# Kernel optimization log

Measured on AMD Instinct MI355X. Metric: run time of the kernel, lower is better.

The kernel has to match this reference:

```python
import jax, jax.numpy as jnp
import numpy as np

ROPE_BASE = 10000.0


def _apply_rope(q, k, start_pos):
    # q, k: (B, T, H, D) with half-split (LLaMA-style) rotation
    B, T, H, D = q.shape
    half = D // 2
    inv_freq = 1.0 / (ROPE_BASE ** (jnp.arange(0, half, dtype=jnp.float32) / half))
    pos = (start_pos + jnp.arange(T)).astype(jnp.float32)
    ang = pos[:, None] * inv_freq[None, :]          # (T, half)
    cos = jnp.cos(ang)[None, :, None, :]            # (1, T, 1, half)
    sin = jnp.sin(ang)[None, :, None, :]

    def rot(t):
        t1, t2 = t[..., :half], t[..., half:]
        return jnp.concatenate([t1 * cos - t2 * sin, t1 * sin + t2 * cos], axis=-1)

    return rot(q), rot(k)


def setup_inputs() -> dict:
    key = jax.random.key(0)
    k1, k2, k3 = jax.random.split(key, 3)
    B, T, C = 2, 2048, 2048
    x = jax.random.normal(k1, (B, T, C), dtype=jnp.float32)
    # torch Linear weights: (out_features, in_features), scaled like default init
    Wqkv = jax.random.normal(k2, (3 * C, C), dtype=jnp.float32) * (C ** -0.5)
    Wproj = jax.random.normal(k3, (C, C), dtype=jnp.float32) * (C ** -0.5)
    return {"x": x, "Wqkv": Wqkv, "Wproj": Wproj, "start_pos": 0}


def reference(x, Wqkv, Wproj, start_pos):
    B, T, C = x.shape
    H = 16
    D = C // H
    scale = D ** -0.5

    qkv = x @ Wqkv.T                                 # (B, T, 3C)
    q, k, v = jnp.split(qkv, 3, axis=-1)
    q = q.reshape(B, T, H, D)
    k = k.reshape(B, T, H, D)
    v = v.reshape(B, T, H, D)
    q, k = _apply_rope(q, k, start_pos)

    att = jnp.einsum("bthd,bshd->bhts", q, k) * scale   # (B, H, T, T)
    causal = jnp.tril(jnp.ones((T, T), dtype=bool))
    att = jnp.where(causal[None, None], att, -jnp.inf)
    att = jax.nn.softmax(att, axis=-1)
    out = jnp.einsum("bhts,bshd->bthd", att, v)          # (B, T, H, D)
    out = out.reshape(B, T, C)
    return out @ Wproj.T
```

## Files before the change

kernel.cpp:

```cpp
#include <hip/hip_runtime.h>
#include <hip/hip_bf16.h>
#include <stdint.h>
#include <math.h>

#define B_    2
#define T_    2048
#define C_    2048
#define H_    16
#define D_    128
#define NQKV  6144
#define BT_   4096

typedef __attribute__((ext_vector_type(8))) short  short8;
typedef __attribute__((ext_vector_type(4))) short  short4_;
typedef __attribute__((ext_vector_type(4))) float  float4_;

__device__ __forceinline__ unsigned short f2bf(float f) {
  union { float f; unsigned int u; } v; v.f = f;
  unsigned int u = v.u;
  return (unsigned short)((u + 0x7FFFu + ((u >> 16) & 1u)) >> 16);
}
__device__ __forceinline__ float bf2f(unsigned short u) {
  union { unsigned int i; float f; } v; v.i = ((unsigned int)u) << 16;
  return v.f;
}
__device__ __forceinline__ void pk2(short4_& dst, int idx2, float a, float b) {
  union { __hip_bfloat162 h2; struct { short x, y; } s; } u;
  u.h2 = __float22bfloat162_rn(make_float2(a, b));
  dst[idx2 * 2]     = u.s.x;
  dst[idx2 * 2 + 1] = u.s.y;
}

__device__ __forceinline__ void async_cp16(const unsigned short* g, unsigned short* l) {
  __builtin_amdgcn_global_load_lds((__attribute__((address_space(1))) void*)g,
                                   (__attribute__((address_space(3))) void*)l,
                                   16, 0, 0);
}

__global__ __launch_bounds__(256) void cvt_all(const float* __restrict__ x,
                                               const float* __restrict__ wqkv,
                                               const float* __restrict__ wproj,
                                               unsigned short* __restrict__ out) {
  int i = (blockIdx.x * 256 + threadIdx.x) * 8;
  const float* src; int off;
  if (i < 8388608)       { src = x;     off = i; }
  else if (i < 20971520) { src = wqkv;  off = i - 8388608; }
  else                   { src = wproj; off = i - 20971520; }
  const float4_* p = (const float4_*)(src + off);
  float4_ a = p[0], b = p[1];
  short8 o;
  o[0] = (short)f2bf(a[0]); o[1] = (short)f2bf(a[1]);
  o[2] = (short)f2bf(a[2]); o[3] = (short)f2bf(a[3]);
  o[4] = (short)f2bf(b[0]); o[5] = (short)f2bf(b[1]);
  o[6] = (short)f2bf(b[2]); o[7] = (short)f2bf(b[3]);
  *(short8*)(out + i) = o;
}

template <bool F32OUT>
__global__ __launch_bounds__(256) void gemm_bt(const unsigned short* __restrict__ A,
                                               const unsigned short* __restrict__ Bm,
                                               void* __restrict__ Cout,
                                               int M, int N, int K) {
  __shared__ __align__(16) unsigned short As[128 * 64];
  __shared__ __align__(16) unsigned short Bs[128 * 64];
  const int tid  = threadIdx.x;
  const int lane = tid & 63;
  const int col16 = lane & 15, quad = lane >> 4;
  const int wave = tid >> 6;
  const int wm = wave >> 1, wn = wave & 1;
  const int m0 = blockIdx.y * 128, n0 = blockIdx.x * 128;

  float4_ acc[4][4] = {};

  #pragma unroll 1
  for (int k0 = 0; k0 < K; k0 += 64) {
    __syncthreads();
    #pragma unroll
    for (int i = 0; i < 4; ++i) {
      int P   = i * 256 + tid;
      int row = P >> 3;
      int kc  = (P & 7) ^ (row & 7);
      async_cp16(A  + (size_t)(m0 + row) * K + k0 + kc * 8, As + P * 8);
      async_cp16(Bm + (size_t)(n0 + row) * K + k0 + kc * 8, Bs + P * 8);
    }
    __syncthreads();
    #pragma unroll
    for (int ks = 0; ks < 2; ++ks) {
      short8 af[4], bf[4];
      #pragma unroll
      for (int i = 0; i < 4; ++i) {
        int ra = wm * 64 + i * 16 + col16;
        int ca = ((ks * 4 + quad) ^ (ra & 7)) * 8;
        af[i] = *(const short8*)(As + ra * 64 + ca);
        int rb = wn * 64 + i * 16 + col16;
        int cb = ((ks * 4 + quad) ^ (rb & 7)) * 8;
        bf[i] = *(const short8*)(Bs + rb * 64 + cb);
      }
      #pragma unroll
      for (int i = 0; i < 4; ++i)
        #pragma unroll
        for (int j = 0; j < 4; ++j)
          acc[i][j] = __builtin_amdgcn_mfma_f32_16x16x32_bf16(af[i], bf[j], acc[i][j], 0, 0, 0);
    }
  }

  #pragma unroll
  for (int i = 0; i < 4; ++i) {
    int mg = m0 + wm * 64 + i * 16 + quad * 4;
    #pragma unroll
    for (int j = 0; j < 4; ++j) {
      int ng = n0 + wn * 64 + j * 16 + col16;
      #pragma unroll
      for (int r = 0; r < 4; ++r) {
        if constexpr (F32OUT)
          ((float*)Cout)[(size_t)(mg + r) * N + ng] = acc[i][j][r];
        else
          ((unsigned short*)Cout)[(size_t)(mg + r) * N + ng] = f2bf(acc[i][j][r]);
      }
    }
  }
}

__global__ __launch_bounds__(256) void rope_split(const unsigned short* __restrict__ qkv,
                                                  const int* __restrict__ sp_ptr,
                                                  unsigned short* __restrict__ q_r,
                                                  unsigned short* __restrict__ k_r,
                                                  unsigned short* __restrict__ v_t) {
  __shared__ __align__(16) unsigned short vs[128 * 64];
  const int blk  = blockIdx.x;
  const int bh   = blk >> 5;
  const int tile = blk & 31;
  const int b = bh >> 4, h = bh & 15;
  const int t0 = tile * 64;
  const int tid = threadIdx.x;
  const int qidx = tid & 15;
  const int sp = sp_ptr[0];
  const bool hi = (qidx & 8) != 0;
  const float L2F = -0.20762050593046013f;
  const float SCL = 0.1275174117f;

  #pragma unroll
  for (int p = 0; p < 4; ++p) {
    int row = p * 16 + (tid >> 4);
    int tg  = t0 + row;
    size_t base = (size_t)(b * T_ + tg) * NQKV + h * D_ + qidx * 8;
    short8 q8 = *(const short8*)(qkv + base);
    short8 k8 = *(const short8*)(qkv + base + 2048);
    short8 v8 = *(const short8*)(qkv + base + 4096);
    float qf[8], kf[8], qp[8], kp[8];
    #pragma unroll
    for (int j = 0; j < 8; ++j) { qf[j] = bf2f((unsigned short)q8[j]); kf[j] = bf2f((unsigned short)k8[j]); }
    #pragma unroll
    for (int j = 0; j < 8; ++j) { qp[j] = __shfl_xor(qf[j], 8); kp[j] = __shfl_xor(kf[j], 8); }
    float pos = (float)(sp + tg);
    short8 qo, ko;
    #pragma unroll
    for (int j = 0; j < 8; ++j) {
      int d  = qidx * 8 + j;
      int fi = d & 63;
      float freq = exp2f((float)fi * L2F);
      float ang = pos * freq;
      float s = sinf(ang), c = cosf(ang);
      float sq = s * SCL, cq = c * SCL;
      float o1 = hi ? (qp[j] * sq + qf[j] * cq) : (qf[j] * cq - qp[j] * sq);
      float o2 = hi ? (kp[j] * s  + kf[j] * c ) : (kf[j] * c  - kp[j] * s );
      qo[j] = (short)f2bf(o1);
      ko[j] = (short)f2bf(o2);
    }
    size_t ob = (size_t)(bh * T_ + tg) * D_ + qidx * 8;
    *(short8*)(q_r + ob) = qo;
    *(short8*)(k_r + ob) = ko;
    #pragma unroll
    for (int j = 0; j < 8; ++j) {
      int d  = qidx * 8 + j;
      int prc = (row >> 3) ^ ((d >> 3) & 7);
      vs[d * 64 + prc * 8 + (row & 7)] = (unsigned short)v8[j];
    }
  }
  __syncthreads();
  int drow = tid >> 1;
  int half = tid & 1;
  size_t gb = (size_t)(bh * D_ + drow) * T_ + t0 + half * 32;
  #pragma unroll
  for (int c = 0; c < 4; ++c) {
    int rc  = half * 4 + c;
    int prc = rc ^ ((drow >> 3) & 7);
    *(short8*)(v_t + gb + c * 8) = *(const short8*)(vs + drow * 64 + prc * 8);
  }
}

__global__ __launch_bounds__(512) void attn_fwd(const unsigned short* __restrict__ q_r,
                                                const unsigned short* __restrict__ k_r,
                                                const unsigned short* __restrict__ v_t,
                                                unsigned short* __restrict__ Ob) {
  __shared__ __align__(16) unsigned short Ks[2][64 * 128];
  __shared__ __align__(16) unsigned short Vts[2][128 * 64];
  __shared__ __align__(16) unsigned short Ps[128 * 64];
  const int pairb = blockIdx.x >> 5;
  const int bh    = blockIdx.x & 31;
  const int tid  = threadIdx.x;
  const int lane = tid & 63;
  const int col16 = lane & 15, quad = lane >> 4;
  const int wave = tid >> 6;
  const float NEG_INF = -__builtin_inff();
  const int b = bh >> 4, h = bh & 15;
  const int qlr = wave * 16 + col16;

  #pragma unroll 1
  for (int half = 0; half < 2; ++half) {
    const int qt = half ? (15 - pairb) : pairb;
    const int q0 = qt * 128;
    const int njt = 2 * qt + 2;

    short8 qf[4];
    const unsigned short* qp = q_r + (size_t)(bh * T_ + q0 + qlr) * D_;
    #pragma unroll
    for (int ks = 0; ks < 4; ++ks) qf[ks] = *(const short8*)(qp + ks * 32 + quad * 8);

    float4_ oacc[8] = {};
    float m_i = NEG_INF, l_i = 0.f;

    __syncthreads();

    const unsigned short* kbase = k_r + (size_t)bh * T_ * D_;
    const unsigned short* vbase = v_t + (size_t)bh * D_ * T_;
    #define STAGE(JT, BUF)                                                        \
      {                                                                           \
        const unsigned short* kb = kbase + (size_t)(JT) * 64 * D_;                \
        const unsigned short* vb = vbase + (size_t)(JT) * 64;                     \
        unsigned short* kd = &Ks[(BUF)][0];                                       \
        unsigned short* vd = &Vts[(BUF)][0];                                      \
        _Pragma("unroll")                                                         \
        for (int i = 0; i < 2; ++i) {                                             \
          int P = i * 512 + tid;                                                  \
          int krow = P >> 4, kc = (P & 15) ^ (krow & 7);                          \
          async_cp16(kb + krow * D_ + kc * 8, kd + P * 8);                        \
          int vrow = P >> 3, vc = (P & 7) ^ (vrow & 7);                           \
          async_cp16(vb + (size_t)vrow * T_ + vc * 8, vd + P * 8);                \
        }                                                                         \
      }

    STAGE(0, 0);

    #pragma unroll 1
    for (int jt = 0; jt < njt; ++jt) {
      __syncthreads();
      if (jt + 1 < njt) STAGE(jt + 1, (jt + 1) & 1);

      if (jt * 64 > q0 + wave * 16 + 15) continue;

      const unsigned short* KsB  = &Ks[jt & 1][0];
      const unsigned short* VtsB = &Vts[jt & 1][0];

      float4_ s[4];
      #pragma unroll
      for (int jn = 0; jn < 4; ++jn) {
        float4_ a = {};
        #pragma unroll
        for (int ks = 0; ks < 4; ++ks) {
          int kr = jn * 16 + col16;
          int ch = ((ks * 4 + quad) ^ (kr & 7)) * 8;
          short8 kfr = *(const short8*)(KsB + kr * 128 + ch);
          a = __builtin_amdgcn_mfma_f32_16x16x32_bf16(kfr, qf[ks], a, 0, 0, 0);
        }
        s[jn] = a;
      }
      if (jt * 64 + 63 > q0 + wave * 16) {
        #pragma unroll
        for (int jn = 0; jn < 4; ++jn)
          #pragma unroll
          for (int r = 0; r < 4; ++r)
            if (jt * 64 + jn * 16 + quad * 4 + r > q0 + qlr) s[jn][r] = NEG_INF;
      }
      float rm = NEG_INF;
      #pragma unroll
      for (int jn = 0; jn < 4; ++jn)
        #pragma unroll
        for (int r = 0; r < 4; ++r) rm = fmaxf(rm, s[jn][r]);
      rm = fmaxf(rm, __shfl_xor(rm, 16));
      rm = fmaxf(rm, __shfl_xor(rm, 32));
      float m_new = fmaxf(m_i, rm);
      float alpha = exp2f(m_i - m_new);
      float rs = 0.f;
      #pragma unroll
      for (int jn = 0; jn < 4; ++jn)
        #pragma unroll
        for (int r = 0; r < 4; ++r) {
          float pv = exp2f(s[jn][r] - m_new);
          s[jn][r] = pv;
          rs += pv;
        }
      rs += __shfl_xor(rs, 16);
      rs += __shfl_xor(rs, 32);
      l_i = l_i * alpha + rs;
      m_i = m_new;
      #pragma unroll
      for (int dt = 0; dt < 8; ++dt) oacc[dt] *= alpha;

      #pragma unroll
      for (int jn = 0; jn < 4; ++jn) {
        short4_ pkv;
        pk2(pkv, 0, s[jn][0], s[jn][1]);
        pk2(pkv, 1, s[jn][2], s[jn][3]);
        int c0 = jn * 16 + quad * 4;
        int ch = (c0 >> 3) ^ (qlr & 7);
        *(short4_*)(Ps + qlr * 64 + ch * 8 + (c0 & 7)) = pkv;
      }
      __builtin_amdgcn_s_waitcnt(0xC07F);

      short8 pf[2];
      #pragma unroll
      for (int ks2 = 0; ks2 < 2; ++ks2) {
        int ch = ((ks2 * 4 + quad) ^ (qlr & 7)) * 8;
        pf[ks2] = *(const short8*)(Ps + qlr * 64 + ch);
      }
      #pragma unroll
      for (int dt = 0; dt < 8; ++dt)
        #pragma unroll
        for (int ks2 = 0; ks2 < 2; ++ks2) {
          int vr = dt * 16 + col16;
          int ch = ((ks2 * 4 + quad) ^ (vr & 7)) * 8;
          short8 vf = *(const short8*)(VtsB + vr * 64 + ch);
          oacc[dt] = __builtin_amdgcn_mfma_f32_16x16x32_bf16(vf, pf[ks2], oacc[dt], 0, 0, 0);
        }
    }

    float inv_l = 1.0f / l_i;
    size_t ob = (size_t)(b * T_ + q0 + qlr) * C_ + h * D_;
    #pragma unroll
    for (int dt = 0; dt < 8; ++dt) {
      short4_ o4;
      pk2(o4, 0, oacc[dt][0] * inv_l, oacc[dt][1] * inv_l);
      pk2(o4, 1, oacc[dt][2] * inv_l, oacc[dt][3] * inv_l);
      *(short4_*)(Ob + ob + dt * 16 + quad * 4) = o4;
    }
    #undef STAGE
  }
}

extern "C" void kernel_launch(void* const* d_in, const int* in_sizes, int n_in,
                              void* d_out, int out_size, void* d_ws, size_t ws_size,
                              hipStream_t stream) {
  const float* x     = (const float*)d_in[0];
  const float* Wqkv  = (const float*)d_in[1];
  const float* Wproj = (const float*)d_in[2];
  const int*   sp    = (const int*)d_in[3];
  float* out = (float*)d_out;

  unsigned short* ws     = (unsigned short*)d_ws;
  unsigned short* xb     = ws;
  unsigned short* wqkvb  = xb + 8388608;
  unsigned short* wprojb = wqkvb + 12582912;
  unsigned short* qkvb   = wprojb + 4194304;
  unsigned short* q_r    = qkvb + 25165824;
  unsigned short* k_r    = q_r + 8388608;
  unsigned short* v_t    = k_r + 8388608;
  unsigned short* Obuf   = xb;

  cvt_all<<<25165824 / 2048, 256, 0, stream>>>(x, Wqkv, Wproj, ws);

  gemm_bt<false><<<dim3(48, 32), 256, 0, stream>>>(xb, wqkvb, (void*)qkvb, BT_, NQKV, C_);

  rope_split<<<1024, 256, 0, stream>>>(qkvb, sp, q_r, k_r, v_t);

  attn_fwd<<<dim3(256), 512, 0, stream>>>(q_r, k_r, v_t, Obuf);

  gemm_bt<true><<<dim3(16, 32), 256, 0, stream>>>(Obuf, wprojb, (void*)out, BT_, C_, C_);
}
```

Baseline: 387.2 us.

## Add 256x256-tile 8-wave pipelined GEMM for QKV projection

Replaces the QKV projection GEMM with a new kernel that uses 256x256 output tiles, 8 waves per block and double-buffered async global-to-LDS copies. Each K tile is split into four phases that interleave the staging of upcoming tiles with MFMA work, using explicit barriers, waitcnt and setprio. Blocks are remapped across 8 groups, likely to spread work over the XCDs. This aims to raise data reuse and hide memory latency in the largest GEMM, in exchange for higher register and LDS pressure and fragile hand-placed synchronisation.

```diff
diff --git a/kernel.cpp b/kernel.cpp
--- a/kernel.cpp
+++ b/kernel.cpp
@@ -121,6 +121,122 @@
   }
 }
 
+__global__ __launch_bounds__(512, 2) void gemm_bt_8ph(const unsigned short* __restrict__ A,
+                                                      const unsigned short* __restrict__ Bm,
+                                                      unsigned short* __restrict__ Cout,
+                                                      int M, int N, int K) {
+  __shared__ __align__(16) unsigned short As[2][2][8192];
+  __shared__ __align__(16) unsigned short Bs[2][2][8192];
+
+  const int tid   = threadIdx.x;
+  const int lane  = tid & 63;
+  const int col16 = lane & 15, quad = lane >> 4;
+  const int wave  = tid >> 6;
+  const int wm = wave >> 2;
+  const int wn = wave & 3;
+
+  const int nby = M >> 8, nwg = gridDim.x, q = nwg >> 3;
+  const int wg = (blockIdx.x & 7) * q + (blockIdx.x >> 3);
+  const int by = wg % nby, bx = wg / nby;
+  const int m0 = by * 256, n0 = bx * 256;
+
+  const int nkt = K >> 6;
+
+  const int kc0 = (tid & 3) ^ ((tid >> 3) & 3);
+  const size_t soff = (size_t)(tid >> 2) * K + kc0 * 8;
+  const unsigned short* Ab = A  + (size_t)m0 * K;
+  const unsigned short* Bb = Bm + (size_t)n0 * K;
+
+  const int swz  = quad ^ ((col16 >> 1) & 3);
+  const int aidx = (wm * 128 + col16) * 32 + swz * 8;
+  const int bidx = (wn * 64  + col16) * 32 + swz * 8;
+
+  float4_ acc[8][4] = {};
+  short8 af[4], bfr[4];
+
+#define STAGEH(GB, LB)                                                         \
+  {                                                                            \
+    const unsigned short* g_ = (GB);                                           \
+    async_cp16(g_,                  (LB) + tid * 8);                           \
+    async_cp16(g_ + 128 * (size_t)K, (LB) + 4096 + tid * 8);                   \
+  }
+
+#define PHASE(BUF, MH, KS, DO_B, STG, DO_VM)                                   \
+  {                                                                            \
+    const unsigned short* ap_ = &As[BUF][KS][0] + aidx + (MH) * 2048;          \
+    af[0] = *(const short8*)(ap_);                                             \
+    af[1] = *(const short8*)(ap_ + 512);                                       \
+    af[2] = *(const short8*)(ap_ + 1024);                                      \
+    af[3] = *(const short8*)(ap_ + 1536);                                      \
+    if (DO_B) {                                                                \
+      const unsigned short* bp_ = &Bs[BUF][KS][0] + bidx;                      \
+      bfr[0] = *(const short8*)(bp_);                                          \
+      bfr[1] = *(const short8*)(bp_ + 512);                                    \
+      bfr[2] = *(const short8*)(bp_ + 1024);                                   \
+      bfr[3] = *(const short8*)(bp_ + 1536);                                   \
+    }                                                                          \
+    STG;                                                                       \
+    __builtin_amdgcn_s_barrier();                                              \
+    asm volatile("s_waitcnt lgkmcnt(0)" ::: "memory");                         \
+    __builtin_amdgcn_sched_barrier(0);                                         \
+    __builtin_amdgcn_s_setprio(1);                                             \
+    _Pragma("unroll")                                                          \
+    for (int mi_ = 0; mi_ < 4; ++mi_)                                          \
+      _Pragma("unroll")                                                        \
+      for (int ni_ = 0; ni_ < 4; ++ni_)                                        \
+        acc[(MH) * 4 + mi_][ni_] = __builtin_amdgcn_mfma_f32_16x16x32_bf16(    \
+            af[mi_], bfr[ni_], acc[(MH) * 4 + mi_][ni_], 0, 0, 0);             \
+    __builtin_amdgcn_s_setprio(0);                                             \
+    if (DO_VM) {                                                               \
+      asm volatile("s_waitcnt vmcnt(8)" ::: "memory");                         \
+      __builtin_amdgcn_sched_barrier(0);                                       \
+    }                                                                          \
+    __builtin_amdgcn_s_barrier();                                              \
+  }
+
+#define TILE(KT, BUF)                                                          \
+  {                                                                            \
+    const int t1_ = (KT) + 1 < nkt ? (KT) + 1 : nkt - 1;                       \
+    const int t2_ = (KT) + 2 < nkt ? (KT) + 2 : nkt - 1;                       \
+    const int k1_ = t1_ * 64, k2_ = t2_ * 64;                                  \
+    PHASE(BUF, 0, 0, 1, STAGEH(Ab + soff + k1_ + 32, &As[1 - (BUF)][1][0]), 0) \
+    PHASE(BUF, 1, 0, 0, STAGEH(Bb + soff + k1_ + 32, &Bs[1 - (BUF)][1][0]), 1) \
+    PHASE(BUF, 0, 1, 1, STAGEH(Ab + soff + k2_,      &As[BUF][0][0]),       0) \
+    PHASE(BUF, 1, 1, 0, STAGEH(Bb + soff + k2_,      &Bs[BUF][0][0]),       1) \
+  }
+
+  STAGEH(Ab + soff,      &As[0][0][0]);
+  STAGEH(Bb + soff,      &Bs[0][0][0]);
+  STAGEH(Ab + soff + 32, &As[0][1][0]);
+  STAGEH(Bb + soff + 32, &Bs[0][1][0]);
+  STAGEH(Ab + soff + 64, &As[1][0][0]);
+  STAGEH(Bb + soff + 64, &Bs[1][0][0]);
+  asm volatile("s_waitcnt vmcnt(8)" ::: "memory");
+  __builtin_amdgcn_sched_barrier(0);
+  __builtin_amdgcn_s_barrier();
+
+  #pragma unroll 1
+  for (int kt = 0; kt < nkt; kt += 2) {
+    TILE(kt, 0)
+    TILE(kt + 1, 1)
+  }
+#undef TILE
+#undef PHASE
+#undef STAGEH
+
+  #pragma unroll
+  for (int mi = 0; mi < 8; ++mi) {
+    int mg = m0 + wm * 128 + mi * 16 + quad * 4;
+    #pragma unroll
+    for (int ni = 0; ni < 4; ++ni) {
+      int ng = n0 + wn * 64 + ni * 16 + col16;
+      #pragma unroll
+      for (int r = 0; r < 4; ++r)
+        Cout[(size_t)(mg + r) * N + ng] = f2bf(acc[mi][ni][r]);
+    }
+  }
+}
+
 __global__ __launch_bounds__(256) void rope_split(const unsigned short* __restrict__ qkv,
                                                   const int* __restrict__ sp_ptr,
                                                   unsigned short* __restrict__ q_r,
@@ -359,7 +475,7 @@
 
   cvt_all<<<25165824 / 2048, 256, 0, stream>>>(x, Wqkv, Wproj, ws);
 
-  gemm_bt<false><<<dim3(48, 32), 256, 0, stream>>>(xb, wqkvb, (void*)qkvb, BT_, NQKV, C_);
+  gemm_bt_8ph<<<dim3(384), 512, 0, stream>>>(xb, wqkvb, qkvb, BT_, NQKV, C_);
 
   rope_split<<<1024, 256, 0, stream>>>(qkvb, sp, q_r, k_r, v_t);
 
```

Measured after the change: 394.8 us. About the same (+2.0%).

## Fuse RoPE, head split and V transpose into QKV GEMM epilogue

Applied to the files above, without the earlier changes.

Replaces the generic QKV GEMM plus separate rope_split kernel with a dedicated GEMM whose epilogue applies RoPE (with the softmax scale folded into Q) and writes Q/K in per-head layout, or transposes V through shared memory into v_t. Each 128-column tile maps to exactly one head of Q, K or V, and the B-tile rows are remapped so each wave holds matching lo/hi halves of the head dimension. This removes the intermediate qkv buffer round trip and one kernel launch. In exchange the epilogue does per-element sin/cos and scattered 2-byte stores.

```diff
diff --git a/kernel.cpp b/kernel.cpp
--- a/kernel.cpp
+++ b/kernel.cpp
@@ -121,71 +121,110 @@
   }
 }
 
-__global__ __launch_bounds__(256) void rope_split(const unsigned short* __restrict__ qkv,
-                                                  const int* __restrict__ sp_ptr,
-                                                  unsigned short* __restrict__ q_r,
-                                                  unsigned short* __restrict__ k_r,
-                                                  unsigned short* __restrict__ v_t) {
-  __shared__ __align__(16) unsigned short vs[128 * 64];
-  const int blk  = blockIdx.x;
-  const int bh   = blk >> 5;
-  const int tile = blk & 31;
-  const int b = bh >> 4, h = bh & 15;
-  const int t0 = tile * 64;
-  const int tid = threadIdx.x;
-  const int qidx = tid & 15;
-  const int sp = sp_ptr[0];
-  const bool hi = (qidx & 8) != 0;
+__global__ __launch_bounds__(256) void gemm_qkv(const unsigned short* __restrict__ A,
+                                                const unsigned short* __restrict__ Bm,
+                                                const int* __restrict__ sp_ptr,
+                                                unsigned short* __restrict__ q_r,
+                                                unsigned short* __restrict__ k_r,
+                                                unsigned short* __restrict__ v_t) {
+  __shared__ __align__(16) unsigned short S[16384];
+  unsigned short* As = S;
+  unsigned short* Bs = S + 8192;
+  const int tid  = threadIdx.x;
+  const int lane = tid & 63;
+  const int col16 = lane & 15, quad = lane >> 4;
+  const int wave = tid >> 6;
+  const int wm = wave >> 1, wn = wave & 1;
+  const int m0 = blockIdx.y * 128, n0 = blockIdx.x * 128;
+
+  float4_ acc[4][4] = {};
+
+  #pragma unroll 1
+  for (int k0 = 0; k0 < C_; k0 += 64) {
+    __syncthreads();
+    #pragma unroll
+    for (int i = 0; i < 4; ++i) {
+      int P   = i * 256 + tid;
+      int row = P >> 3;
+      int kc  = (P & 7) ^ (row & 7);
+      async_cp16(A  + (size_t)(m0 + row) * C_ + k0 + kc * 8, As + P * 8);
+      async_cp16(Bm + (size_t)(n0 + row) * C_ + k0 + kc * 8, Bs + P * 8);
+    }
+    __syncthreads();
+    #pragma unroll
+    for (int ks = 0; ks < 2; ++ks) {
+      short8 af[4], bf[4];
+      #pragma unroll
+      for (int i = 0; i < 4; ++i) {
+        int ra = wm * 64 + i * 16 + col16;
+        int ca = ((ks * 4 + quad) ^ (ra & 7)) * 8;
+        af[i] = *(const short8*)(As + ra * 64 + ca);
+        int rb = wn * 32 + (i & 1) * 16 + (i >> 1) * 64 + col16;
+        int cb = ((ks * 4 + quad) ^ (rb & 7)) * 8;
+        bf[i] = *(const short8*)(Bs + rb * 64 + cb);
+      }
+      #pragma unroll
+      for (int i = 0; i < 4; ++i)
+        #pragma unroll
+        for (int j = 0; j < 4; ++j)
+          acc[i][j] = __builtin_amdgcn_mfma_f32_16x16x32_bf16(af[i], bf[j], acc[i][j], 0, 0, 0);
+    }
+  }
+
+  const int region = n0 >> 11;
+  const int h   = (n0 & 2047) >> 7;
+  const int b   = m0 >> 11;
+  const int t0l = m0 & 2047;
+  const int bh  = b * H_ + h;
   const float L2F = -0.20762050593046013f;
-  const float SCL = 0.1275174117f;
-
-  #pragma unroll
-  for (int p = 0; p < 4; ++p) {
-    int row = p * 16 + (tid >> 4);
-    int tg  = t0 + row;
-    size_t base = (size_t)(b * T_ + tg) * NQKV + h * D_ + qidx * 8;
-    short8 q8 = *(const short8*)(qkv + base);
-    short8 k8 = *(const short8*)(qkv + base + 2048);
-    short8 v8 = *(const short8*)(qkv + base + 4096);
-    float qf[8], kf[8], qp[8], kp[8];
-    #pragma unroll
-    for (int j = 0; j < 8; ++j) { qf[j] = bf2f((unsigned short)q8[j]); kf[j] = bf2f((unsigned short)k8[j]); }
-    #pragma unroll
-    for (int j = 0; j < 8; ++j) { qp[j] = __shfl_xor(qf[j], 8); kp[j] = __shfl_xor(kf[j], 8); }
-    float pos = (float)(sp + tg);
-    short8 qo, ko;
-    #pragma unroll
-    for (int j = 0; j < 8; ++j) {
-      int d  = qidx * 8 + j;
-      int fi = d & 63;
-      float freq = exp2f((float)fi * L2F);
-      float ang = pos * freq;
-      float s = sinf(ang), c = cosf(ang);
-      float sq = s * SCL, cq = c * SCL;
-      float o1 = hi ? (qp[j] * sq + qf[j] * cq) : (qf[j] * cq - qp[j] * sq);
-      float o2 = hi ? (kp[j] * s  + kf[j] * c ) : (kf[j] * c  - kp[j] * s );
-      qo[j] = (short)f2bf(o1);
-      ko[j] = (short)f2bf(o2);
-    }
-    size_t ob = (size_t)(bh * T_ + tg) * D_ + qidx * 8;
-    *(short8*)(q_r + ob) = qo;
-    *(short8*)(k_r + ob) = ko;
-    #pragma unroll
-    for (int j = 0; j < 8; ++j) {
-      int d  = qidx * 8 + j;
-      int prc = (row >> 3) ^ ((d >> 3) & 7);
-      vs[d * 64 + prc * 8 + (row & 7)] = (unsigned short)v8[j];
-    }
-  }
-  __syncthreads();
-  int drow = tid >> 1;
-  int half = tid & 1;
-  size_t gb = (size_t)(bh * D_ + drow) * T_ + t0 + half * 32;
-  #pragma unroll
-  for (int c = 0; c < 4; ++c) {
-    int rc  = half * 4 + c;
-    int prc = rc ^ ((drow >> 3) & 7);
-    *(short8*)(v_t + gb + c * 8) = *(const short8*)(vs + drow * 64 + prc * 8);
+
+  if (region < 2) {
+    unsigned short* dst = region ? k_r : q_r;
+    const float scl = region ? 1.0f : 0.1275174117f;
+    const int sp = sp_ptr[0];
+    #pragma unroll
+    for (int i = 0; i < 4; ++i) {
+      int tl = t0l + wm * 64 + i * 16 + quad * 4;
+      #pragma unroll
+      for (int jl = 0; jl < 2; ++jl) {
+        int d = wn * 32 + jl * 16 + col16;
+        float fr = exp2f((float)d * L2F);
+        size_t ob = (size_t)(bh * T_ + tl) * D_ + d;
+        #pragma unroll
+        for (int r = 0; r < 4; ++r) {
+          float pos = (float)(sp + tl + r);
+          float ang = pos * fr;
+          float sn = sinf(ang), cs = cosf(ang);
+          float lo = acc[i][jl][r], hi = acc[i][jl + 2][r];
+          dst[ob + (size_t)r * D_]      = f2bf((lo * cs - hi * sn) * scl);
+          dst[ob + (size_t)r * D_ + 64] = f2bf((lo * sn + hi * cs) * scl);
+        }
+      }
+    }
+  } else {
+    __syncthreads();
+    #pragma unroll
+    for (int i = 0; i < 4; ++i) {
+      int tlb = wm * 64 + i * 16 + quad * 4;
+      #pragma unroll
+      for (int j = 0; j < 4; ++j) {
+        int d = wn * 32 + (j & 1) * 16 + (j >> 1) * 64 + col16;
+        #pragma unroll
+        for (int r = 0; r < 4; ++r) {
+          int t = tlb + r;
+          int ch = (t >> 3) ^ (d & 15);
+          S[d * 128 + ch * 8 + (t & 7)] = f2bf(acc[i][j][r]);
+        }
+      }
+    }
+    __syncthreads();
+    int drow = tid >> 1, hf = tid & 1;
+    size_t gb = (size_t)(bh * D_ + drow) * T_ + t0l + hf * 64;
+    #pragma unroll
+    for (int cc = 0; cc < 8; ++cc) {
+      int ch = (hf * 8 + cc) ^ (drow & 15);
+      *(short8*)(v_t + gb + cc * 8) = *(const short8*)(S + drow * 128 + ch * 8);
+    }
   }
 }
 
@@ -351,17 +390,14 @@
   unsigned short* xb     = ws;
   unsigned short* wqkvb  = xb + 8388608;
   unsigned short* wprojb = wqkvb + 12582912;
-  unsigned short* qkvb   = wprojb + 4194304;
-  unsigned short* q_r    = qkvb + 25165824;
+  unsigned short* q_r    = wprojb + 4194304;
   unsigned short* k_r    = q_r + 8388608;
   unsigned short* v_t    = k_r + 8388608;
   unsigned short* Obuf   = xb;
 
   cvt_all<<<25165824 / 2048, 256, 0, stream>>>(x, Wqkv, Wproj, ws);
 
-  gemm_bt<false><<<dim3(48, 32), 256, 0, stream>>>(xb, wqkvb, (void*)qkvb, BT_, NQKV, C_);
-
-  rope_split<<<1024, 256, 0, stream>>>(qkvb, sp, q_r, k_r, v_t);
+  gemm_qkv<<<dim3(48, 32), 256, 0, stream>>>(xb, wqkvb, sp, q_r, k_r, v_t);
 
   attn_fwd<<<dim3(256), 512, 0, stream>>>(q_r, k_r, v_t, Obuf);
 
```

Result: slower. 1.361 ms (+251.4%).
